# Performance work log

Hardware: AMD Instinct MI355X
Metric: run time of the kernel (lower is better)

## Reference

```python
import jax, jax.numpy as jnp
import numpy as np

N_STACK = 12
ZERO_OFFSET = 0.001
EPS = 1e-8  # torch cosine_similarity eps


def cos_sim_vec_batch(a, b):
    """torch.cosine_similarity(a[None], b, dim=1): a [V], b [B,V] -> [B]."""
    na = jnp.maximum(jnp.sqrt(jnp.sum(a * a)), EPS)
    nb = jnp.maximum(jnp.sqrt(jnp.sum(b * b, axis=-1)), EPS)
    return (b @ a) / (na * nb)


def setup_inputs() -> dict:
    key = jax.random.key(0)
    k1, k2, k3, k4 = jax.random.split(key, 4)
    B, S, V = 64, 256, 2048
    return {
        "x": jax.random.normal(k1, (B, S, V), dtype=jnp.float32),
        "latch_init": jax.random.normal(k2, (B, V), dtype=jnp.float32),
        "should_pop": jax.random.normal(k3, (V,), dtype=jnp.float32),
        "sharpen_pointer": jnp.ones((1,), dtype=jnp.float32) * 5.0,
        "latch_enable": jax.random.normal(k4, (V,), dtype=jnp.float32) * 0.01,
    }


def reference(x, latch_init, should_pop, sharpen_pointer, latch_enable):
    B, S, V = x.shape
    sharpen = sharpen_pointer[0]
    # Stack state: stack [B, N, V] filled with zero_offset, pointer one-hot at slot 0.
    stack0 = jnp.full((B, N_STACK, V), ZERO_OFFSET, dtype=x.dtype)
    pointer0 = jnp.zeros((B, N_STACK), dtype=x.dtype).at[:, 0].set(1.0)

    def step(carry, inp):
        stack, pointer, latch = carry
        # per-step latch gating -> pop strength (dropout p=0.02 is identity in eval)
        pop = jax.nn.elu(cos_sim_vec_batch(should_pop, latch))  # [B]
        push = 1.0 - pop
        nop = jnp.zeros_like(pop)
        # sharpen the pointer, read the value that would be popped
        psharp = jax.nn.softmax(pointer * sharpen, axis=1)           # [B, N]
        pop_val = jnp.einsum('bnv,bn->bv', stack, psharp)
        # push branch: advance pointer, write value at new top
        push_p = jnp.roll(psharp, 1, axis=1)
        push_stack = stack * (1.0 - push_p[..., None]) + inp[:, None, :] * push_p[..., None]
        # pop branch: erase top back to zero_offset, retreat pointer
        pop_p = jnp.roll(psharp, -1, axis=1)
        pop_stack = stack * (1.0 - psharp[..., None]) + ZERO_OFFSET * psharp[..., None]
        # superposition of the three ops weighted by (push, pop, nop)
        new_stack = (push[:, None, None] * push_stack
                     + pop[:, None, None] * pop_stack
                     + nop[:, None, None] * stack)
        new_pointer = (push[:, None] * push_p
                       + pop[:, None] * pop_p
                       + nop[:, None] * psharp)
        # read stack top, gate by pop strength
        top = jnp.einsum('bnv,bn->bv', new_stack, new_pointer)      # [B, V]
        out = pop[:, None] * top
        # DataLatch update: interp by cosine sim of enable param with enable input
        e = cos_sim_vec_batch(latch_enable, inp)                     # [B]
        new_latch = (1.0 - e)[:, None] * latch + e[:, None] * inp
        return (new_stack, new_pointer, new_latch), (out, new_latch, pop, top)

    x_t = jnp.swapaxes(x, 0, 1)  # [S, B, V]
    _, (outs, latches, pops, tops) = jax.lax.scan(step, (stack0, pointer0, latch_init), x_t)
    outputs = jnp.swapaxes(outs, 0, 1)       # [B, S, V]
    latch_states = jnp.swapaxes(latches, 0, 1)
    pops_out = jnp.swapaxes(pops, 0, 1)       # [B, S]
    stack_tops = jnp.swapaxes(tops, 0, 1)
    return outputs, latch_states, pops_out, stack_tops
```

## Files before the change

### kernel.cpp

```cpp
#include <hip/hip_runtime.h>
#include <math.h>

#define B_ 64
#define S_ 256
#define V_ 2048
#define NS 12
#define ZOFF 0.001f
#define EPSF 1e-8f
#define EPS2 1e-16f
#define NCHS 32

#define WS_NSP2 0
#define WS_D0   64
#define WS_N0   128
#define WS_E    256
#define WS_R    (WS_E + B_*S_)
#define WS_NX2  (WS_R + B_*S_)
#define WS_H    (WS_NX2 + B_*S_)

typedef float f32x4 __attribute__((ext_vector_type(4)));

template<int CTRL>
__device__ __forceinline__ float dpp_mov(float x) {
    return __int_as_float(__builtin_amdgcn_update_dpp(
        0, __float_as_int(x), CTRL, 0xf, 0xf, true));
}

__device__ __forceinline__ float row16_sum(float x) {
    x += dpp_mov<0x121>(x);
    x += dpp_mov<0x122>(x);
    x += dpp_mov<0x124>(x);
    x += dpp_mov<0x128>(x);
    return x;
}

__device__ __forceinline__ float wave_sum64_fast(float x) {
    x = row16_sum(x);
    x += __shfl_xor(x, 16);
    x += __shfl_xor(x, 32);
    return x;
}

__device__ __forceinline__ void ntstore4(float* p, f32x4 v) {
    __builtin_nontemporal_store(v, (f32x4*)p);
}

__global__ void __launch_bounds__(256) k_e(const float* __restrict__ x,
                                           const float* __restrict__ le,
                                           const float* __restrict__ sp,
                                           const float* __restrict__ l0,
                                           float* __restrict__ ws) {
    int blk = blockIdx.x;
    int tid = threadIdx.x;
    int wave = tid >> 6, lane = tid & 63;
    __shared__ float red4[4][4];
    if (blk >= B_ * S_) {
        int nb = blk - B_ * S_;
        float a = 0.f, b = 0.f;
        if (nb == 0) {
            for (int i = tid; i < V_; i += 256) { float y = sp[i]; a += y * y; }
        } else {
            const float* lr = l0 + (size_t)(nb - 1) * V_;
            for (int i = tid; i < V_; i += 256) {
                float l = lr[i], s = sp[i];
                a += s * l; b += l * l;
            }
        }
        a = wave_sum64_fast(a); b = wave_sum64_fast(b);
        if (lane == 0) { red4[wave][0] = a; red4[wave][1] = b; }
        __syncthreads();
        if (tid == 0) {
            float s0 = red4[0][0] + red4[1][0] + red4[2][0] + red4[3][0];
            float s1 = red4[0][1] + red4[1][1] + red4[2][1] + red4[3][1];
            if (nb == 0) ws[WS_NSP2] = s0;
            else { ws[WS_D0 + nb - 1] = s0; ws[WS_N0 + nb - 1] = s1; }
        }
        return;
    }
    int bt = blk;
    const float4* xb = (const float4*)(x + (size_t)bt * V_);
    const float4* le4 = (const float4*)le;
    const float4* sp4 = (const float4*)sp;
    float dot = 0.f, nx = 0.f, rr = 0.f, nle = 0.f;
#pragma unroll
    for (int k = 0; k < 2; k++) {
        int i = tid + k * 256;
        float4 xv = xb[i], lv = le4[i], sv = sp4[i];
        dot += xv.x * lv.x + xv.y * lv.y + xv.z * lv.z + xv.w * lv.w;
        nx  += xv.x * xv.x + xv.y * xv.y + xv.z * xv.z + xv.w * xv.w;
        rr  += xv.x * sv.x + xv.y * sv.y + xv.z * sv.z + xv.w * sv.w;
        nle += lv.x * lv.x + lv.y * lv.y + lv.z * lv.z + lv.w * lv.w;
    }
    dot = wave_sum64_fast(dot); nx = wave_sum64_fast(nx);
    rr = wave_sum64_fast(rr);   nle = wave_sum64_fast(nle);
    if (lane == 0) {
        red4[wave][0] = dot; red4[wave][1] = nx;
        red4[wave][2] = rr;  red4[wave][3] = nle;
    }
    __syncthreads();
    if (tid == 0) {
        float d  = red4[0][0] + red4[1][0] + red4[2][0] + red4[3][0];
        float n  = red4[0][1] + red4[1][1] + red4[2][1] + red4[3][1];
        float r  = red4[0][2] + red4[1][2] + red4[2][2] + red4[3][2];
        float nl = red4[0][3] + red4[1][3] + red4[2][3] + red4[3][3];
        ws[WS_E + bt]   = d * __frsqrt_rn(fmaxf(nl, EPS2)) * __frsqrt_rn(fmaxf(n, EPS2));
        ws[WS_R + bt]   = r;
        ws[WS_NX2 + bt] = n;
    }
}

__global__ void __launch_bounds__(64) k_latch(const float* __restrict__ x,
                        const float* __restrict__ latch_init,
                        float* __restrict__ latch_out,
                        float* __restrict__ ws) {
    int c = blockIdx.x, b = blockIdx.y;
    int lane = threadIdx.x;
    int v = c * 64 + lane;

    __shared__ float se[S_];
    for (int t = lane; t < S_; t += 64) se[t] = ws[WS_E + b * S_ + t];
    __syncthreads();

    float latch = latch_init[(size_t)b * V_ + v];
    const float* xb = x + (size_t)b * S_ * V_ + v;
    float* lo = latch_out + (size_t)b * S_ * V_ + v;
    float* hpp = ws + WS_H + (size_t)(b * NCHS + c) * S_ * 4;
    bool hwr = (lane & 15) == 0;
    int hq = lane >> 4;

    auto step = [&](int t, float xv, float e) {
        float rs = row16_sum(latch * xv);
        if (hwr) hpp[t * 4 + hq] = rs;
        latch = fmaf(e, xv - latch, latch);
        __builtin_nontemporal_store(latch, lo + (size_t)t * V_);
    };

    float xc[8]; float ec[8];
#pragma unroll
    for (int k = 0; k < 8; k++) { xc[k] = xb[(size_t)k * V_]; ec[k] = se[k]; }
    for (int t = 0; t < S_; t += 8) {
        float y[8], f[8];
        if (t + 8 < S_) {
#pragma unroll
            for (int k = 0; k < 8; k++) {
                y[k] = xb[(size_t)(t + 8 + k) * V_];
                f[k] = se[t + 8 + k];
            }
        } else {
#pragma unroll
            for (int k = 0; k < 8; k++) { y[k] = 0.f; f[k] = 0.f; }
        }
#pragma unroll
        for (int k = 0; k < 8; k++) step(t + k, xc[k], ec[k]);
#pragma unroll
        for (int k = 0; k < 8; k++) { xc[k] = y[k]; ec[k] = f[k]; }
    }
}

template<bool UP>
__device__ __forceinline__ void fused_loop(
    int lane, float kq, float inv_nsp, float d, float n,
    const float* __restrict__ sh, const float* __restrict__ se_,
    const float* __restrict__ sr_, const float* __restrict__ snx_,
    float* __restrict__ slot0, float* __restrict__ slot1,
    const float* __restrict__ xp, float* __restrict__ op,
    float* __restrict__ tp, float* __restrict__ pops_b, bool wrpops)
{
    bool act = lane < NS, is0 = (lane == 0), is11 = (lane == 11);
    float p = is0 ? 1.f : 0.f;

    auto chain_step = [&](int t, float* slot) {
        float e = se_[t], r = sr_[t], hh = sh[t], xx = snx_[t];
        float cs = d * inv_nsp * __frsqrt_rn(fmaxf(n, EPS2));
        float pop = cs > 0.f ? cs : __expf(cs) - 1.f;
        float push = 1.f - pop;
        float ez = act ? exp2f(p * kq) : 0.f;
        float s = row16_sum(ez);
        float psh = ez * __frcp_rn(s);
        float fm = UP ? dpp_mov<0x12F>(psh) : dpp_mov<0x121>(psh);
        float fp = UP ? dpp_mov<0x121>(psh) : dpp_mov<0x12F>(psh);
        float wm = UP ? dpp_mov<0x12B>(psh) : dpp_mov<0x125>(psh);
        float wp = UP ? dpp_mov<0x125>(psh) : dpp_mov<0x12B>(psh);
        float push_p = is0  ? wm : fm;
        float pop_p  = is11 ? wp : fp;
        float bb = push * push_p;
        float cc = pop * psh;
        float a  = 1.f - bb - cc;
        float pnew = fmaf(pop, pop_p, bb);
        float4 cv = act ? make_float4(a, bb, cc * ZOFF, pnew)
                        : make_float4(pop, 0.f, 0.f, 0.f);
        if (lane <= NS) *(float4*)(slot + lane * 4) = cv;
        if (wrpops && lane == 0) pops_b[t] = pop;
        p = pnew;
        float om = 1.f - e;
        d = fmaf(om, d, e * r);
        n = fmaf(om * om, n, fmaf(2.f * e * om, hh, e * e * xx));
    };

    f32x4 st[NS];
#pragma unroll
    for (int i = 0; i < NS; i++) st[i] = (f32x4){ZOFF, ZOFF, ZOFF, ZOFF};

    auto scan_step = [&](const float* cf, int t, f32x4 xv) {
        f32x4 top = (f32x4){0.f, 0.f, 0.f, 0.f};
#pragma unroll
        for (int i = 0; i < NS; i++) {
            float4 c4 = *(const float4*)(cf + i * 4);
            f32x4 bx;
            bx.x = fmaf(c4.y, xv.x, c4.z);
            bx.y = fmaf(c4.y, xv.y, c4.z);
            bx.z = fmaf(c4.y, xv.z, c4.z);
            bx.w = fmaf(c4.y, xv.w, c4.z);
            st[i].x = fmaf(c4.x, st[i].x, bx.x);
            st[i].y = fmaf(c4.x, st[i].y, bx.y);
            st[i].z = fmaf(c4.x, st[i].z, bx.z);
            st[i].w = fmaf(c4.x, st[i].w, bx.w);
            top.x = fmaf(c4.w, st[i].x, top.x);
            top.y = fmaf(c4.w, st[i].y, top.y);
            top.z = fmaf(c4.w, st[i].z, top.z);
            top.w = fmaf(c4.w, st[i].w, top.w);
        }
        float pop = cf[48];
        ntstore4(tp + (size_t)t * V_, top);
        f32x4 ot = {pop * top.x, pop * top.y, pop * top.z, pop * top.w};
        ntstore4(op + (size_t)t * V_, ot);
    };

    chain_step(0, slot0);
    f32x4 xc[8];
#pragma unroll
    for (int k = 0; k < 8; k++) xc[k] = *(const f32x4*)(xp + (size_t)k * V_);
    for (int t = 0; t < S_; t += 8) {
        f32x4 y[8];
        if (t + 8 < S_) {
#pragma unroll
            for (int k = 0; k < 8; k++) y[k] = *(const f32x4*)(xp + (size_t)(t + 8 + k) * V_);
        } else {
#pragma unroll
            for (int k = 0; k < 8; k++) y[k] = (f32x4){0.f, 0.f, 0.f, 0.f};
        }
#pragma unroll
        for (int k = 0; k < 8; k++) {
            int tt = t + k;
            if (tt + 1 < S_) chain_step(tt + 1, ((tt + 1) & 1) ? slot1 : slot0);
            scan_step((tt & 1) ? slot1 : slot0, tt, xc[k]);
        }
#pragma unroll
        for (int k = 0; k < 8; k++) xc[k] = y[k];
    }
}

__global__ void __launch_bounds__(128) k_stackptr(const float* __restrict__ sharpen_ptr,
                                                  const float* __restrict__ x,
                                                  float* __restrict__ ws,
                                                  float* __restrict__ pops_out,
                                                  float* __restrict__ outputs,
                                                  float* __restrict__ tops) {
    int b = blockIdx.y, ch = blockIdx.x;
    int tid = threadIdx.x;
    int w = tid >> 6, lane = tid & 63;
    __shared__ float sh[S_], se_[S_], sr_[S_], snx_[S_];
    __shared__ float scoef[2][2][52];

    const float4* hp4 = (const float4*)(ws + WS_H) + (size_t)b * NCHS * S_;
    for (int t = tid; t < S_; t += 128) {
        float h = 0.f;
#pragma unroll
        for (int c = 0; c < NCHS; c++) {
            float4 vv = hp4[(size_t)c * S_ + t];
            h += (vv.x + vv.y) + (vv.z + vv.w);
        }
        sh[t] = h;
        se_[t]  = ws[WS_E + b * S_ + t];
        sr_[t]  = ws[WS_R + b * S_ + t];
        snx_[t] = ws[WS_NX2 + b * S_ + t];
    }
    __syncthreads();

    float kq = sharpen_ptr[0] * 1.44269504f;
    float inv_nsp = 1.f / fmaxf(sqrtf(ws[WS_NSP2]), EPSF);
    float d0 = ws[WS_D0 + b];
    float n0 = ws[WS_N0 + b];

    int v = ch * 512 + w * 256 + lane * 4;
    const float* xp = x + (size_t)b * S_ * V_ + v;
    float* op = outputs + (size_t)b * S_ * V_ + v;
    float* tp = tops + (size_t)b * S_ * V_ + v;
    float* pops_b = pops_out + (size_t)b * S_;
    bool wrpops = (ch == 0 && w == 0);

    float pw = dpp_mov<0x121>((float)lane);
    bool up = (__builtin_amdgcn_readlane(__float_as_int(pw), 0) == __float_as_int(1.0f));
    if (up) fused_loop<true>(lane, kq, inv_nsp, d0, n0, sh, se_, sr_, snx_,
                             &scoef[w][0][0], &scoef[w][1][0], xp, op, tp, pops_b, wrpops);
    else    fused_loop<false>(lane, kq, inv_nsp, d0, n0, sh, se_, sr_, snx_,
                              &scoef[w][0][0], &scoef[w][1][0], xp, op, tp, pops_b, wrpops);
}

extern "C" void kernel_launch(void* const* d_in, const int* in_sizes, int n_in,
                              void* d_out, int out_size, void* d_ws, size_t ws_size,
                              hipStream_t stream) {
    const float* x           = (const float*)d_in[0];
    const float* latch_init  = (const float*)d_in[1];
    const float* should_pop  = (const float*)d_in[2];
    const float* sharpen_ptr = (const float*)d_in[3];
    const float* latch_en    = (const float*)d_in[4];

    float* out = (float*)d_out;
    const size_t BSV = (size_t)B_ * S_ * V_;
    float* outputs      = out;
    float* latch_states = out + BSV;
    float* pops         = out + 2 * BSV;
    float* tops         = out + 2 * BSV + (size_t)B_ * S_;
    float* ws = (float*)d_ws;

    k_e<<<B_ * S_ + 1 + B_, 256, 0, stream>>>(x, latch_en, should_pop, latch_init, ws);
    k_latch<<<dim3(NCHS, B_), 64, 0, stream>>>(x, latch_init, latch_states, ws);
    k_stackptr<<<dim3(4, B_), 128, 0, stream>>>(sharpen_ptr, x, ws, pops, outputs, tops);
}
```

Before: 197.1 us.

## Split stack scan across four waves per block with two elements per lane

```diff
diff --git a/kernel.cpp b/kernel.cpp
--- a/kernel.cpp
+++ b/kernel.cpp
@@ -41,8 +41,9 @@
     return x;
 }
 
-__device__ __forceinline__ void ntstore4(float* p, f32x4 v) {
-    __builtin_nontemporal_store(v, (f32x4*)p);
+__device__ __forceinline__ void ntstore2(float2* p, float a, float b) {
+    float2 v = make_float2(a, b);
+    __builtin_nontemporal_store(__builtin_bit_cast(double, v), (double*)p);
 }
 
 __global__ void __launch_bounds__(256) k_e(const float* __restrict__ x,
@@ -163,11 +164,12 @@
     const float* __restrict__ sh, const float* __restrict__ se_,
     const float* __restrict__ sr_, const float* __restrict__ snx_,
     float* __restrict__ slot0, float* __restrict__ slot1,
-    const float* __restrict__ xp, float* __restrict__ op,
-    float* __restrict__ tp, float* __restrict__ pops_b, bool wrpops)
+    const float2* __restrict__ xp, float2* __restrict__ op,
+    float2* __restrict__ tp, float* __restrict__ pops_b, bool wrpops)
 {
     bool act = lane < NS, is0 = (lane == 0), is11 = (lane == 11);
     float p = is0 ? 1.f : 0.f;
+    const int VS = V_ / 2;
 
     auto chain_step = [&](int t, float* slot) {
         float e = se_[t], r = sr_[t], hh = sh[t], xx = snx_[t];
@@ -197,47 +199,39 @@
         n = fmaf(om * om, n, fmaf(2.f * e * om, hh, e * e * xx));
     };
 
-    f32x4 st[NS];
-#pragma unroll
-    for (int i = 0; i < NS; i++) st[i] = (f32x4){ZOFF, ZOFF, ZOFF, ZOFF};
-
-    auto scan_step = [&](const float* cf, int t, f32x4 xv) {
-        f32x4 top = (f32x4){0.f, 0.f, 0.f, 0.f};
+    float st0[NS], st1[NS];
+#pragma unroll
+    for (int i = 0; i < NS; i++) { st0[i] = ZOFF; st1[i] = ZOFF; }
+
+    auto scan_step = [&](const float* cf, int t, float2 xv) {
+        float top0 = 0.f, top1 = 0.f;
 #pragma unroll
         for (int i = 0; i < NS; i++) {
             float4 c4 = *(const float4*)(cf + i * 4);
-            f32x4 bx;
-            bx.x = fmaf(c4.y, xv.x, c4.z);
-            bx.y = fmaf(c4.y, xv.y, c4.z);
-            bx.z = fmaf(c4.y, xv.z, c4.z);
-            bx.w = fmaf(c4.y, xv.w, c4.z);
-            st[i].x = fmaf(c4.x, st[i].x, bx.x);
-            st[i].y = fmaf(c4.x, st[i].y, bx.y);
-            st[i].z = fmaf(c4.x, st[i].z, bx.z);
-            st[i].w = fmaf(c4.x, st[i].w, bx.w);
-            top.x = fmaf(c4.w, st[i].x, top.x);
-            top.y = fmaf(c4.w, st[i].y, top.y);
-            top.z = fmaf(c4.w, st[i].z, top.z);
-            top.w = fmaf(c4.w, st[i].w, top.w);
+            float bx0 = fmaf(c4.y, xv.x, c4.z);
+            float bx1 = fmaf(c4.y, xv.y, c4.z);
+            st0[i] = fmaf(c4.x, st0[i], bx0);
+            st1[i] = fmaf(c4.x, st1[i], bx1);
+            top0 = fmaf(c4.w, st0[i], top0);
+            top1 = fmaf(c4.w, st1[i], top1);
         }
         float pop = cf[48];
-        ntstore4(tp + (size_t)t * V_, top);
-        f32x4 ot = {pop * top.x, pop * top.y, pop * top.z, pop * top.w};
-        ntstore4(op + (size_t)t * V_, ot);
+        ntstore2(tp + (size_t)t * VS, top0, top1);
+        ntstore2(op + (size_t)t * VS, pop * top0, pop * top1);
     };
 
     chain_step(0, slot0);
-    f32x4 xc[8];
-#pragma unroll
-    for (int k = 0; k < 8; k++) xc[k] = *(const f32x4*)(xp + (size_t)k * V_);
+    float2 xc[8];
+#pragma unroll
+    for (int k = 0; k < 8; k++) xc[k] = xp[(size_t)k * VS];
     for (int t = 0; t < S_; t += 8) {
-        f32x4 y[8];
+        float2 y[8];
         if (t + 8 < S_) {
 #pragma unroll
-            for (int k = 0; k < 8; k++) y[k] = *(const f32x4*)(xp + (size_t)(t + 8 + k) * V_);
+            for (int k = 0; k < 8; k++) y[k] = xp[(size_t)(t + 8 + k) * VS];
         } else {
 #pragma unroll
-            for (int k = 0; k < 8; k++) y[k] = (f32x4){0.f, 0.f, 0.f, 0.f};
+            for (int k = 0; k < 8; k++) y[k] = make_float2(0.f, 0.f);
         }
 #pragma unroll
         for (int k = 0; k < 8; k++) {
@@ -250,7 +244,7 @@
     }
 }
 
-__global__ void __launch_bounds__(128) k_stackptr(const float* __restrict__ sharpen_ptr,
+__global__ void __launch_bounds__(256) k_stackptr(const float* __restrict__ sharpen_ptr,
                                                   const float* __restrict__ x,
                                                   float* __restrict__ ws,
                                                   float* __restrict__ pops_out,
@@ -260,10 +254,10 @@
     int tid = threadIdx.x;
     int w = tid >> 6, lane = tid & 63;
     __shared__ float sh[S_], se_[S_], sr_[S_], snx_[S_];
-    __shared__ float scoef[2][2][52];
+    __shared__ float scoef[4][2][52];
 
     const float4* hp4 = (const float4*)(ws + WS_H) + (size_t)b * NCHS * S_;
-    for (int t = tid; t < S_; t += 128) {
+    for (int t = tid; t < S_; t += 256) {
         float h = 0.f;
 #pragma unroll
         for (int c = 0; c < NCHS; c++) {
@@ -282,10 +276,10 @@
     float d0 = ws[WS_D0 + b];
     float n0 = ws[WS_N0 + b];
 
-    int v = ch * 512 + w * 256 + lane * 4;
-    const float* xp = x + (size_t)b * S_ * V_ + v;
-    float* op = outputs + (size_t)b * S_ * V_ + v;
-    float* tp = tops + (size_t)b * S_ * V_ + v;
+    int v = ch * 512 + w * 128 + lane * 2;
+    const float2* xp = (const float2*)(x + (size_t)b * S_ * V_ + v);
+    float2* op = (float2*)(outputs + (size_t)b * S_ * V_ + v);
+    float2* tp = (float2*)(tops + (size_t)b * S_ * V_ + v);
     float* pops_b = pops_out + (size_t)b * S_;
     bool wrpops = (ch == 0 && w == 0);
 
@@ -316,5 +310,5 @@
 
     k_e<<<B_ * S_ + 1 + B_, 256, 0, stream>>>(x, latch_en, should_pop, latch_init, ws);
     k_latch<<<dim3(NCHS, B_), 64, 0, stream>>>(x, latch_init, latch_states, ws);
-    k_stackptr<<<dim3(4, B_), 128, 0, stream>>>(sharpen_ptr, x, ws, pops, outputs, tops);
-}
+    k_stackptr<<<dim3(4, B_), 256, 0, stream>>>(sharpen_ptr, x, ws, pops, outputs, tops);
+}
```

Result: no change. 198.8 us (+0.8%).

## Split pointer chain and stack scan into producer/consumer warps

Applied to the files above, without the earlier changes.

```diff
diff --git a/kernel.cpp b/kernel.cpp
--- a/kernel.cpp
+++ b/kernel.cpp
@@ -158,18 +158,18 @@
 }
 
 template<bool UP>
-__device__ __forceinline__ void fused_loop(
-    int lane, float kq, float inv_nsp, float d, float n,
+__device__ __forceinline__ void chain_chunk(
+    int lane, float kq, float inv_nsp,
+    float& p, float& d, float& n,
     const float* __restrict__ sh, const float* __restrict__ se_,
     const float* __restrict__ sr_, const float* __restrict__ snx_,
-    float* __restrict__ slot0, float* __restrict__ slot1,
-    const float* __restrict__ xp, float* __restrict__ op,
-    float* __restrict__ tp, float* __restrict__ pops_b, bool wrpops)
+    float* __restrict__ buf, int t0,
+    float* __restrict__ pops_b, bool wrpops)
 {
     bool act = lane < NS, is0 = (lane == 0), is11 = (lane == 11);
-    float p = is0 ? 1.f : 0.f;
-
-    auto chain_step = [&](int t, float* slot) {
+#pragma unroll 4
+    for (int k = 0; k < 32; ++k) {
+        int t = t0 + k;
         float e = se_[t], r = sr_[t], hh = sh[t], xx = snx_[t];
         float cs = d * inv_nsp * __frsqrt_rn(fmaxf(n, EPS2));
         float pop = cs > 0.f ? cs : __expf(cs) - 1.f;
@@ -189,68 +189,16 @@
         float pnew = fmaf(pop, pop_p, bb);
         float4 cv = act ? make_float4(a, bb, cc * ZOFF, pnew)
                         : make_float4(pop, 0.f, 0.f, 0.f);
-        if (lane <= NS) *(float4*)(slot + lane * 4) = cv;
+        if (lane <= NS) *(float4*)(buf + k * 52 + lane * 4) = cv;
         if (wrpops && lane == 0) pops_b[t] = pop;
         p = pnew;
         float om = 1.f - e;
         d = fmaf(om, d, e * r);
         n = fmaf(om * om, n, fmaf(2.f * e * om, hh, e * e * xx));
-    };
-
-    f32x4 st[NS];
-#pragma unroll
-    for (int i = 0; i < NS; i++) st[i] = (f32x4){ZOFF, ZOFF, ZOFF, ZOFF};
-
-    auto scan_step = [&](const float* cf, int t, f32x4 xv) {
-        f32x4 top = (f32x4){0.f, 0.f, 0.f, 0.f};
-#pragma unroll
-        for (int i = 0; i < NS; i++) {
-            float4 c4 = *(const float4*)(cf + i * 4);
-            f32x4 bx;
-            bx.x = fmaf(c4.y, xv.x, c4.z);
-            bx.y = fmaf(c4.y, xv.y, c4.z);
-            bx.z = fmaf(c4.y, xv.z, c4.z);
-            bx.w = fmaf(c4.y, xv.w, c4.z);
-            st[i].x = fmaf(c4.x, st[i].x, bx.x);
-            st[i].y = fmaf(c4.x, st[i].y, bx.y);
-            st[i].z = fmaf(c4.x, st[i].z, bx.z);
-            st[i].w = fmaf(c4.x, st[i].w, bx.w);
-            top.x = fmaf(c4.w, st[i].x, top.x);
-            top.y = fmaf(c4.w, st[i].y, top.y);
-            top.z = fmaf(c4.w, st[i].z, top.z);
-            top.w = fmaf(c4.w, st[i].w, top.w);
-        }
-        float pop = cf[48];
-        ntstore4(tp + (size_t)t * V_, top);
-        f32x4 ot = {pop * top.x, pop * top.y, pop * top.z, pop * top.w};
-        ntstore4(op + (size_t)t * V_, ot);
-    };
-
-    chain_step(0, slot0);
-    f32x4 xc[8];
-#pragma unroll
-    for (int k = 0; k < 8; k++) xc[k] = *(const f32x4*)(xp + (size_t)k * V_);
-    for (int t = 0; t < S_; t += 8) {
-        f32x4 y[8];
-        if (t + 8 < S_) {
-#pragma unroll
-            for (int k = 0; k < 8; k++) y[k] = *(const f32x4*)(xp + (size_t)(t + 8 + k) * V_);
-        } else {
-#pragma unroll
-            for (int k = 0; k < 8; k++) y[k] = (f32x4){0.f, 0.f, 0.f, 0.f};
-        }
-#pragma unroll
-        for (int k = 0; k < 8; k++) {
-            int tt = t + k;
-            if (tt + 1 < S_) chain_step(tt + 1, ((tt + 1) & 1) ? slot1 : slot0);
-            scan_step((tt & 1) ? slot1 : slot0, tt, xc[k]);
-        }
-#pragma unroll
-        for (int k = 0; k < 8; k++) xc[k] = y[k];
-    }
-}
-
-__global__ void __launch_bounds__(128) k_stackptr(const float* __restrict__ sharpen_ptr,
+    }
+}
+
+__global__ void __launch_bounds__(192) k_stackptr(const float* __restrict__ sharpen_ptr,
                                                   const float* __restrict__ x,
                                                   float* __restrict__ ws,
                                                   float* __restrict__ pops_out,
@@ -258,12 +206,12 @@
                                                   float* __restrict__ tops) {
     int b = blockIdx.y, ch = blockIdx.x;
     int tid = threadIdx.x;
-    int w = tid >> 6, lane = tid & 63;
+    int w = tid / 64, lane = tid % 64;
     __shared__ float sh[S_], se_[S_], sr_[S_], snx_[S_];
-    __shared__ float scoef[2][2][52];
+    __shared__ float scoef[2][32][52];
 
     const float4* hp4 = (const float4*)(ws + WS_H) + (size_t)b * NCHS * S_;
-    for (int t = tid; t < S_; t += 128) {
+    for (int t = tid; t < S_; t += 192) {
         float h = 0.f;
 #pragma unroll
         for (int c = 0; c < NCHS; c++) {
@@ -279,22 +227,88 @@
 
     float kq = sharpen_ptr[0] * 1.44269504f;
     float inv_nsp = 1.f / fmaxf(sqrtf(ws[WS_NSP2]), EPSF);
-    float d0 = ws[WS_D0 + b];
-    float n0 = ws[WS_N0 + b];
-
-    int v = ch * 512 + w * 256 + lane * 4;
-    const float* xp = x + (size_t)b * S_ * V_ + v;
-    float* op = outputs + (size_t)b * S_ * V_ + v;
-    float* tp = tops + (size_t)b * S_ * V_ + v;
-    float* pops_b = pops_out + (size_t)b * S_;
-    bool wrpops = (ch == 0 && w == 0);
-
-    float pw = dpp_mov<0x121>((float)lane);
-    bool up = (__builtin_amdgcn_readlane(__float_as_int(pw), 0) == __float_as_int(1.0f));
-    if (up) fused_loop<true>(lane, kq, inv_nsp, d0, n0, sh, se_, sr_, snx_,
-                             &scoef[w][0][0], &scoef[w][1][0], xp, op, tp, pops_b, wrpops);
-    else    fused_loop<false>(lane, kq, inv_nsp, d0, n0, sh, se_, sr_, snx_,
-                              &scoef[w][0][0], &scoef[w][1][0], xp, op, tp, pops_b, wrpops);
+
+    if (w == 0) {
+        float d = ws[WS_D0 + b];
+        float n = ws[WS_N0 + b];
+        float p = (lane == 0) ? 1.f : 0.f;
+        float* pops_b = pops_out + (size_t)b * S_;
+        bool wrpops = (ch == 0);
+        float pw = dpp_mov<0x121>((float)lane);
+        bool up = (__builtin_amdgcn_readlane(__float_as_int(pw), 0) == __float_as_int(1.0f));
+        for (int c = 0; c <= 8; ++c) {
+            if (c < 8) {
+                if (up) chain_chunk<true>(lane, kq, inv_nsp, p, d, n, sh, se_, sr_, snx_,
+                                          &scoef[c & 1][0][0], c * 32, pops_b, wrpops);
+                else    chain_chunk<false>(lane, kq, inv_nsp, p, d, n, sh, se_, sr_, snx_,
+                                           &scoef[c & 1][0][0], c * 32, pops_b, wrpops);
+            }
+            __syncthreads();
+        }
+    } else {
+        int v = ch * 512 + (w - 1) * 256 + lane * 4;
+        const float* xp = x + (size_t)b * S_ * V_ + v;
+        float* op = outputs + (size_t)b * S_ * V_ + v;
+        float* tp = tops + (size_t)b * S_ * V_ + v;
+
+        f32x4 st[NS];
+#pragma unroll
+        for (int i = 0; i < NS; i++) st[i] = (f32x4){ZOFF, ZOFF, ZOFF, ZOFF};
+
+        auto scan_step = [&](const float* cf, int t, f32x4 xv) {
+            f32x4 top = (f32x4){0.f, 0.f, 0.f, 0.f};
+#pragma unroll
+            for (int i = 0; i < NS; i++) {
+                float4 c4 = *(const float4*)(cf + i * 4);
+                f32x4 bx;
+                bx.x = fmaf(c4.y, xv.x, c4.z);
+                bx.y = fmaf(c4.y, xv.y, c4.z);
+                bx.z = fmaf(c4.y, xv.z, c4.z);
+                bx.w = fmaf(c4.y, xv.w, c4.z);
+                st[i].x = fmaf(c4.x, st[i].x, bx.x);
+                st[i].y = fmaf(c4.x, st[i].y, bx.y);
+                st[i].z = fmaf(c4.x, st[i].z, bx.z);
+                st[i].w = fmaf(c4.x, st[i].w, bx.w);
+                top.x = fmaf(c4.w, st[i].x, top.x);
+                top.y = fmaf(c4.w, st[i].y, top.y);
+                top.z = fmaf(c4.w, st[i].z, top.z);
+                top.w = fmaf(c4.w, st[i].w, top.w);
+            }
+            float pop = cf[48];
+            ntstore4(tp + (size_t)t * V_, top);
+            f32x4 ot = {pop * top.x, pop * top.y, pop * top.z, pop * top.w};
+            ntstore4(op + (size_t)t * V_, ot);
+        };
+
+        f32x4 xc[8];
+#pragma unroll
+        for (int k = 0; k < 8; k++) xc[k] = *(const f32x4*)(xp + (size_t)k * V_);
+
+        __syncthreads();
+        for (int c = 1; c <= 8; ++c) {
+            int t0 = (c - 1) * 32;
+            const float* buf = &scoef[(c - 1) & 1][0][0];
+#pragma unroll
+            for (int g = 0; g < 4; ++g) {
+                int t = t0 + g * 8;
+                f32x4 y[8];
+                if (t + 8 < S_) {
+#pragma unroll
+                    for (int k = 0; k < 8; k++)
+                        y[k] = *(const f32x4*)(xp + (size_t)(t + 8 + k) * V_);
+                } else {
+#pragma unroll
+                    for (int k = 0; k < 8; k++) y[k] = (f32x4){0.f, 0.f, 0.f, 0.f};
+                }
+#pragma unroll
+                for (int k = 0; k < 8; k++)
+                    scan_step(buf + (g * 8 + k) * 52, t + k, xc[k]);
+#pragma unroll
+                for (int k = 0; k < 8; k++) xc[k] = y[k];
+            }
+            __syncthreads();
+        }
+    }
 }
 
 extern "C" void kernel_launch(void* const* d_in, const int* in_sizes, int n_in,
@@ -316,5 +330,5 @@
 
     k_e<<<B_ * S_ + 1 + B_, 256, 0, stream>>>(x, latch_en, should_pop, latch_init, ws);
     k_latch<<<dim3(NCHS, B_), 64, 0, stream>>>(x, latch_init, latch_states, ws);
-    k_stackptr<<<dim3(4, B_), 128, 0, stream>>>(sharpen_ptr, x, ws, pops, outputs, tops);
-}
+    k_stackptr<<<dim3(4, B_), 192, 0, stream>>>(sharpen_ptr, x, ws, pops, outputs, tops);
+}
```

Measured after the change: 163.1 us (median of 2 runs). 1.21x faster.
